# Performance work log

Measured on AMD Instinct MI355X. Metric: run time of the kernel, lower is better.

The kernel has to match this reference:

```python
import jax, jax.numpy as jnp
import numpy as np

B, S, E, N, H = 2, 2048, 2048, 16, 128  # batch, seq, embed, heads, depth


def sine_table(features, length, min_timescale=1.0, max_timescale=10000.0):
    fraction = jnp.arange(0, features, 2, dtype=jnp.float32) / features
    timescale = min_timescale * (max_timescale / min_timescale) ** fraction
    sinusoid_inp = jnp.einsum('i,j->ij', jnp.arange(length, dtype=jnp.float32), 1.0 / timescale,
                              precision=jax.lax.Precision.HIGHEST)
    sinusoid_inp = jnp.concatenate([sinusoid_inp, sinusoid_inp], axis=-1)  # [L, features]
    return jnp.sin(sinusoid_inp), jnp.cos(sinusoid_inp)


def rotate_half(x):
    x1, x2 = jnp.split(x, 2, axis=-1)
    return jnp.concatenate([-x2, x1], axis=-1)


def apply_rotary(q, k, cos, sin):
    # q: [B,S,N,H], k: [B,T,N,H]; cos/sin: [L,H] broadcast over (seq, depth)
    qcos = cos[: q.shape[1]][None, :, None, :]
    qsin = sin[: q.shape[1]][None, :, None, :]
    kcos = cos[: k.shape[1]][None, :, None, :]
    ksin = sin[: k.shape[1]][None, :, None, :]
    return q * qcos + rotate_half(q) * qsin, k * kcos + rotate_half(k) * ksin


def setup_inputs() -> dict:
    key = jax.random.key(0)
    ks = jax.random.split(key, 6)
    scale = 1.0 / np.sqrt(E)
    return {
        'x_q': jax.random.normal(ks[0], (B, S, E), jnp.float32),
        'x_kv': jax.random.normal(ks[1], (B, S, E), jnp.float32),
        'WQ': jax.random.normal(ks[2], (E, N, H), jnp.float32) * scale,
        'WK': jax.random.normal(ks[3], (E, N, H), jnp.float32) * scale,
        'WV': jax.random.normal(ks[4], (E, N, H), jnp.float32) * scale,
        'WO': jax.random.normal(ks[5], (N, H, E), jnp.float32) * scale,
    }


def reference(x_q, x_kv, WQ, WK, WV, WO):
    q = jnp.einsum('bse,enh->bsnh', x_q, WQ)
    k = jnp.einsum('bte,enh->btnh', x_kv, WK)
    v = jnp.einsum('bte,enh->btnh', x_kv, WV)

    sin, cos = sine_table(q.shape[-1], max(q.shape[1], k.shape[1]))
    q, k = apply_rotary(q, k, cos, sin)

    # causal attention bias: [1,1,S,T]
    s_len, t_len = q.shape[1], k.shape[1]
    causal = jnp.arange(s_len)[:, None] >= jnp.arange(t_len)[None, :]
    bias = jnp.where(causal, 0.0, -1e10).astype(jnp.float32)[None, None]

    logits = jnp.einsum('bsnh,btnh->bnst', q, k) / np.sqrt(H) + bias
    probs = jax.nn.softmax(logits, axis=-1)
    a = jnp.einsum('bnst,btnh->bsnh', probs, v)
    o = jnp.einsum('bsnh,nhe->bse', a, WO)
    return o
```

## Files before the change

kernel.cpp:

```cpp
#include <hip/hip_runtime.h>
#include <hip/hip_bf16.h>

typedef __bf16 bf16;
typedef __attribute__((ext_vector_type(8))) __bf16 bf16x8;
typedef __attribute__((ext_vector_type(4))) __bf16 bf16x4;
typedef __attribute__((ext_vector_type(4))) float f32x4;

typedef const __attribute__((address_space(1))) void* gptr_t;
typedef __attribute__((address_space(3))) void* sptr_t;

__device__ __forceinline__ void gload16(const void* g, void* l) {
  __builtin_amdgcn_global_load_lds((gptr_t)g, (sptr_t)l, 16, 0, 0);
}

#define MFMA_BF16(a, b, c) __builtin_amdgcn_mfma_f32_16x16x32_bf16((a), (b), (c), 0, 0, 0)

#define BAR() do { asm volatile("" ::: "memory"); __builtin_amdgcn_s_barrier(); asm volatile("" ::: "memory"); } while (0)

__device__ __forceinline__ int swzb(int l) { return l ^ (((l >> 7) & 7) << 4); }

namespace {
constexpr int kB = 2, kS = 2048, kE = 2048, kN = 16, kH = 128;
constexpr float kScale = 0.08838834764831845f;
constexpr float kLog2e = 1.4426950408889634f;
}

__global__ void k_cvt2(const float* __restrict__ a, const float* __restrict__ b,
                       bf16* __restrict__ oa, bf16* __restrict__ ob) {
  int bid = blockIdx.x;
  const float* in = (bid < 8192) ? a : b;
  bf16* out = (bid < 8192) ? oa : ob;
  int i = (bid & 8191) * 256 + threadIdx.x;
  float4 v = reinterpret_cast<const float4*>(in)[i];
  bf16x4 o = { (bf16)v.x, (bf16)v.y, (bf16)v.z, (bf16)v.w };
  reinterpret_cast<bf16x4*>(out)[i] = o;
}

__global__ void k_tconv4(const float* __restrict__ WQ, const float* __restrict__ WK,
                         const float* __restrict__ WV, const float* __restrict__ WO,
                         bf16* __restrict__ OQ, bf16* __restrict__ OK2,
                         bf16* __restrict__ OV, bf16* __restrict__ OO) {
  __shared__ float tile[64][68];
  int bid = blockIdx.x;
  int sel = bid >> 10;
  const float* in = (sel == 0) ? WQ : (sel == 1) ? WK : (sel == 2) ? WV : WO;
  bf16* out = (sel == 0) ? OQ : (sel == 1) ? OK2 : (sel == 2) ? OV : OO;
  int lb = bid & 1023;
  int bx = lb & 31, by = lb >> 5;
  int r0 = by * 64, c0 = bx * 64;
  int t = threadIdx.x;
  int rr = t >> 4, c4 = (t & 15) * 4;
#pragma unroll
  for (int k = 0; k < 4; ++k) {
    int r = rr + k * 16;
    float4 v = *reinterpret_cast<const float4*>(&in[(size_t)(r0 + r) * 2048 + c0 + c4]);
    tile[r][c4] = v.x; tile[r][c4 + 1] = v.y; tile[r][c4 + 2] = v.z; tile[r][c4 + 3] = v.w;
  }
  __syncthreads();
  int cc0 = t >> 3, r8 = (t & 7) * 8;
#pragma unroll
  for (int k = 0; k < 2; ++k) {
    int cc = cc0 + k * 32;
    bf16x8 o;
#pragma unroll
    for (int j = 0; j < 8; ++j) o[j] = (bf16)tile[r8 + j][cc];
    *reinterpret_cast<bf16x8*>(&out[(size_t)(c0 + cc) * 2048 + r0 + r8]) = o;
  }
}

__global__ void k_vtrans(const bf16* __restrict__ V, bf16* __restrict__ Vt) {
  __shared__ bf16 tile[64][72];
  int bid = blockIdx.x;
  int bn = bid >> 6;
  int s0 = ((bid >> 1) & 31) * 64;
  int h0 = (bid & 1) * 64;
  size_t base = (size_t)bn * kS * kH;
  int t = threadIdx.x;
  int r = t >> 3, c8 = (t & 7) * 8;
#pragma unroll
  for (int k = 0; k < 2; ++k) {
    int rr = r + k * 32;
    *reinterpret_cast<bf16x8*>(&tile[rr][c8]) =
        *reinterpret_cast<const bf16x8*>(&V[base + (size_t)(s0 + rr) * kH + h0 + c8]);
  }
  __syncthreads();
  int hh0 = t >> 3, s8 = (t & 7) * 8;
#pragma unroll
  for (int k = 0; k < 2; ++k) {
    int hh = hh0 + k * 32;
    bf16x8 o;
#pragma unroll
    for (int j = 0; j < 8; ++j) o[j] = tile[s8 + j][hh];
    *reinterpret_cast<bf16x8*>(&Vt[base + (size_t)(h0 + hh) * kS + s0 + s8]) = o;
  }
}

__global__ void k_trig(float* __restrict__ ctab, float* __restrict__ stab) {
  int tid = blockIdx.x * 256 + threadIdx.x;
  int s = tid >> 6, i = tid & 63;
  float inv = exp2f(-(float)i * 0.20762050593046457f);
  float ang = (float)s * inv;
  float sn, cs;
  sincosf(ang, &sn, &cs);
  ctab[tid] = cs;
  stab[tid] = sn;
}

__global__ void k_rope(bf16* __restrict__ Qd, bf16* __restrict__ Kd,
                       const float* __restrict__ ctab, const float* __restrict__ stab) {
  int tid = blockIdx.x * 256 + threadIdx.x;
  int i8 = (tid & 7) * 8;
  int s = (tid >> 3) & (kS - 1);
  int bn = tid >> 14;
  size_t base = ((size_t)bn * kS + s) * kH;
  float4 c0 = *reinterpret_cast<const float4*>(&ctab[(s << 6) + i8]);
  float4 c1 = *reinterpret_cast<const float4*>(&ctab[(s << 6) + i8 + 4]);
  float4 s0 = *reinterpret_cast<const float4*>(&stab[(s << 6) + i8]);
  float4 s1 = *reinterpret_cast<const float4*>(&stab[(s << 6) + i8 + 4]);
  float cs[8] = {c0.x, c0.y, c0.z, c0.w, c1.x, c1.y, c1.z, c1.w};
  float sn[8] = {s0.x, s0.y, s0.z, s0.w, s1.x, s1.y, s1.z, s1.w};
  bf16x8 qlo = *reinterpret_cast<const bf16x8*>(&Qd[base + i8]);
  bf16x8 qhi = *reinterpret_cast<const bf16x8*>(&Qd[base + 64 + i8]);
  bf16x8 klo = *reinterpret_cast<const bf16x8*>(&Kd[base + i8]);
  bf16x8 khi = *reinterpret_cast<const bf16x8*>(&Kd[base + 64 + i8]);
  bf16x8 qlo2, qhi2, klo2, khi2;
#pragma unroll
  for (int j = 0; j < 8; ++j) {
    float q1 = (float)qlo[j], q2 = (float)qhi[j];
    qlo2[j] = (bf16)(q1 * cs[j] - q2 * sn[j]);
    qhi2[j] = (bf16)(q2 * cs[j] + q1 * sn[j]);
    float k1 = (float)klo[j], k2 = (float)khi[j];
    klo2[j] = (bf16)(k1 * cs[j] - k2 * sn[j]);
    khi2[j] = (bf16)(k2 * cs[j] + k1 * sn[j]);
  }
  *reinterpret_cast<bf16x8*>(&Qd[base + i8]) = qlo2;
  *reinterpret_cast<bf16x8*>(&Qd[base + 64 + i8]) = qhi2;
  *reinterpret_cast<bf16x8*>(&Kd[base + i8]) = klo2;
  *reinterpret_cast<bf16x8*>(&Kd[base + 64 + i8]) = khi2;
}


__device__ __forceinline__ void stage_half(const bf16* __restrict__ src, size_t row0,
                                           int k0, char* slot, int t) {
#pragma unroll
  for (int i = 0; i < 2; ++i) {
    int idx = i * 512 + t;
    int d = idx * 16;
    int lb = d ^ (((d >> 7) & 7) << 4);
    int r = lb >> 7;
    int kc = (lb & 127) >> 1;
    gload16(src + (row0 + r) * 2048 + k0 + kc,
            slot + i * 8192 + (t >> 6) * 1024);
  }
}

#define AS1(b)    ((char*)LDS + (b) * 16384)
#define BS1(q, h) ((char*)LDS + 32768 + (q) * 32768 + (h) * 16384)

template <int MODE>
__global__ __launch_bounds__(512, 2) void k_gemm8(const bf16* __restrict__ Aq,
                                                  const bf16* __restrict__ Akv,
                                                  const bf16* __restrict__ Bt,
                                                  void* __restrict__ Cout) {
  constexpr int NTN = (MODE == 0) ? 24 : 8;
  constexpr int NTM = 32;
  constexpr int NT = 32;
  __shared__ __align__(16) char LDS[131072];
  int bid = blockIdx.x;
  constexpr int nblk = NTM * NTN;
  int swz = (bid & 7) * (nblk >> 3) + (bid >> 3);
  int mt = swz / NTN, nt = swz - mt * NTN;
  size_t m0 = (size_t)mt * 128;
  int n0 = nt * 256;
  const bf16* A = (MODE == 0 && nt >= 8) ? Akv : Aq;
  int t = threadIdx.x, wid = t >> 6, lane = t & 63;
  int l16 = lane & 15, lq = lane >> 4;
  int wr = wid >> 2, wc = wid & 3;
  int bhalf = wc >> 1;
  int brow0 = ((wc & 1) << 6) + l16;

  f32x4 acc[4][4] = {};
  bf16x8 af[4], bfr[4];

  stage_half(Bt, (size_t)n0,       0, BS1(0, 0), t);
  stage_half(Bt, (size_t)n0 + 128, 0, BS1(0, 1), t);
  stage_half(A,  m0,               0, AS1(0), t);
  stage_half(Bt, (size_t)n0,      64, BS1(1, 0), t);
  stage_half(Bt, (size_t)n0 + 128, 64, BS1(1, 1), t);
  asm volatile("s_waitcnt vmcnt(4)" ::: "memory");
  BAR();

  int bql = 0;
  for (int kt = 0; kt < NT; ++kt) {
    char* Ab = AS1(kt & 1);
    char* Anb = AS1((kt & 1) ^ 1);
    char* Bb = BS1(bql, bhalf);
    int bq2 = bql + 2; if (bq2 >= 3) bq2 -= 3;
#pragma unroll
    for (int j = 0; j < 4; ++j) {
      int l = (((wr * 4 + j) * 16 + l16) << 7) + (lq << 4);
      af[j] = *(const bf16x8*)(Ab + swzb(l));
    }
#pragma unroll
    for (int nf = 0; nf < 2; ++nf) {
      int l = ((brow0 + nf * 16) << 7) + (lq << 4);
      bfr[nf] = *(const bf16x8*)(Bb + swzb(l));
    }
    if (kt + 1 < NT) stage_half(A, m0, (kt + 1) * 64, Anb, t);
    BAR();
    __builtin_amdgcn_s_setprio(1);
#pragma unroll
    for (int j = 0; j < 4; ++j)
#pragma unroll
      for (int nf = 0; nf < 2; ++nf)
        acc[j][nf] = MFMA_BF16(af[j], bfr[nf], acc[j][nf]);
    __builtin_amdgcn_s_setprio(0);
    BAR();
#pragma unroll
    for (int nf = 0; nf < 2; ++nf) {
      int l = ((brow0 + (nf + 2) * 16) << 7) + (lq << 4);
      bfr[2 + nf] = *(const bf16x8*)(Bb + swzb(l));
    }
    if (kt + 2 < NT) {
      stage_half(Bt, (size_t)n0,       (kt + 2) * 64, BS1(bq2, 0), t);
      stage_half(Bt, (size_t)n0 + 128, (kt + 2) * 64, BS1(bq2, 1), t);
    }
    BAR();
    __builtin_amdgcn_s_setprio(1);
#pragma unroll
    for (int j = 0; j < 4; ++j)
#pragma unroll
      for (int nf = 0; nf < 2; ++nf)
        acc[j][2 + nf] = MFMA_BF16(af[j], bfr[2 + nf], acc[j][2 + nf]);
    __builtin_amdgcn_s_setprio(0);
    BAR();
#pragma unroll
    for (int j = 0; j < 4; ++j) {
      int l = (((wr * 4 + j) * 16 + l16) << 7) + 64 + (lq << 4);
      af[j] = *(const bf16x8*)(Ab + swzb(l));
    }
#pragma unroll
    for (int nf = 0; nf < 2; ++nf) {
      int l = ((brow0 + nf * 16) << 7) + 64 + (lq << 4);
      bfr[nf] = *(const bf16x8*)(Bb + swzb(l));
    }
    BAR();
    __builtin_amdgcn_s_setprio(1);
#pragma unroll
    for (int j = 0; j < 4; ++j)
#pragma unroll
      for (int nf = 0; nf < 2; ++nf)
        acc[j][nf] = MFMA_BF16(af[j], bfr[nf], acc[j][nf]);
    __builtin_amdgcn_s_setprio(0);
    BAR();
#pragma unroll
    for (int nf = 0; nf < 2; ++nf) {
      int l = ((brow0 + (nf + 2) * 16) << 7) + 64 + (lq << 4);
      bfr[2 + nf] = *(const bf16x8*)(Bb + swzb(l));
    }
    BAR();
    __builtin_amdgcn_s_setprio(1);
#pragma unroll
    for (int j = 0; j < 4; ++j)
#pragma unroll
      for (int nf = 0; nf < 2; ++nf)
        acc[j][2 + nf] = MFMA_BF16(af[j], bfr[2 + nf], acc[j][2 + nf]);
    __builtin_amdgcn_s_setprio(0);
    if (kt < NT - 2)       asm volatile("s_waitcnt vmcnt(4)" ::: "memory");
    else if (kt == NT - 2) asm volatile("s_waitcnt vmcnt(0)" ::: "memory");
    BAR();
    bql += 1; if (bql >= 3) bql -= 3;
  }

#pragma unroll
  for (int mf = 0; mf < 4; ++mf) {
    int rowb = (int)m0 + wr * 64 + mf * 16 + lq * 4;
#pragma unroll
    for (int nf = 0; nf < 4; ++nf) {
      int col = n0 + wc * 64 + nf * 16 + l16;
#pragma unroll
      for (int r = 0; r < 4; ++r) {
        float v = acc[mf][nf][r];
        int mrow = rowb + r;
        if (MODE == 0) {
          int grp = col >> 11, cw = col & 2047;
          int b = mrow >> 11, s = mrow & 2047, n = cw >> 7, h = cw & 127;
          ((bf16*)Cout)[(size_t)grp * 8388608 +
                        (((size_t)(b * 16 + n) * 2048 + s) << 7) + h] = (bf16)v;
        } else {
          ((float*)Cout)[((size_t)mrow << 11) + col] = v;
        }
      }
    }
  }
}

__global__ __launch_bounds__(512, 4) void k_attn(const bf16* __restrict__ Q,
                                                 const bf16* __restrict__ Kg,
                                                 const bf16* __restrict__ Vt,
                                                 bf16* __restrict__ AO) {
  __shared__ __align__(16) bf16 Ks[64 * 128];
  __shared__ __align__(16) bf16 Vs[128 * 64];
  __shared__ __align__(16) bf16 Ps[8][16][72];
  int bid = blockIdx.x;
  int half = bid >> 8;
  int bn = (half << 4) | ((bid >> 4) & 15);
  int qt = (bid & 15) ^ (half ? 15 : 0);
  int q0 = qt * 128;
  int t = threadIdx.x, wid = t >> 6, lane = t & 63;
  int l16 = lane & 15, lq = lane >> 4;
  size_t bnSH = (size_t)bn * kS * kH;

  int qrow_a = q0 + wid * 16 + l16;
  bf16x8 qf[4];
#pragma unroll
  for (int ks = 0; ks < 4; ++ks)
    qf[ks] = *(const bf16x8*)(Q + bnSH + (size_t)qrow_a * kH + ks * 32 + lq * 8);

  f32x4 oacc[8] = {};
  float mrun[4], lrun[4];
#pragma unroll
  for (int r = 0; r < 4; ++r) { mrun[r] = -1e30f; lrun[r] = 0.f; }

  int ntiles = (q0 + 128) >> 6;
  for (int kt = 0; kt < ntiles; ++kt) {
    int kv0 = kt * 64;
#pragma unroll
    for (int i = 0; i < 2; ++i) {
      int idx = i * 512 + t;
      {
        int row = idx >> 4, ch = idx & 15;
        int gch = ch ^ (row & 7);
        gload16(Kg + bnSH + (size_t)(kv0 + row) * kH + gch * 8,
                (char*)Ks + i * 8192 + wid * 1024);
      }
      {
        int row = idx >> 3, ch = idx & 7;
        int gch = ch ^ (row & 7);
        gload16(Vt + bnSH + (size_t)row * kS + kv0 + gch * 8,
                (char*)Vs + i * 8192 + wid * 1024);
      }
    }
    __syncthreads();

    f32x4 sacc[4] = {};
#pragma unroll
    for (int ks = 0; ks < 4; ++ks) {
#pragma unroll
      for (int ni = 0; ni < 4; ++ni) {
        int sp = ni * 16 + l16;
        int hb = (ks * 32 + lq * 8) * 2;
        bf16x8 kb = *(const bf16x8*)((const char*)Ks + sp * 256 + (hb ^ ((sp & 7) << 4)));
        sacc[ni] = MFMA_BF16(qf[ks], kb, sacc[ni]);
      }
    }

    bool need_mask = (kv0 + 63) > (q0 + wid * 16);
#pragma unroll
    for (int ni = 0; ni < 4; ++ni) {
      f32x4 v = sacc[ni] * kScale;
      if (need_mask) {
#pragma unroll
        for (int r = 0; r < 4; ++r) {
          int qrow = q0 + wid * 16 + lq * 4 + r;
          int col = kv0 + ni * 16 + l16;
          if (col > qrow) v[r] = -1e30f;
        }
      }
      sacc[ni] = v;
    }

    float pmv[4];
#pragma unroll
    for (int r = 0; r < 4; ++r) {
      float pm = fmaxf(fmaxf(sacc[0][r], sacc[1][r]),
                       fmaxf(sacc[2][r], sacc[3][r]));
      pm = fmaxf(pm, __shfl_xor(pm, 1));
      pm = fmaxf(pm, __shfl_xor(pm, 2));
      pm = fmaxf(pm, __shfl_xor(pm, 4));
      pm = fmaxf(pm, __shfl_xor(pm, 8));
      pmv[r] = pm;
    }
    bool growl = (pmv[0] > mrun[0] + 8.f) | (pmv[1] > mrun[1] + 8.f) |
                 (pmv[2] > mrun[2] + 8.f) | (pmv[3] > mrun[3] + 8.f);
    if (__any(growl)) {
#pragma unroll
      for (int r = 0; r < 4; ++r) {
        float mnew = fmaxf(mrun[r], pmv[r]);
        float alpha = exp2f((mrun[r] - mnew) * kLog2e);
        mrun[r] = mnew;
        lrun[r] *= alpha;
#pragma unroll
        for (int nj = 0; nj < 8; ++nj) oacc[nj][r] *= alpha;
      }
    }
#pragma unroll
    for (int r = 0; r < 4; ++r) {
      float rs = 0.f;
#pragma unroll
      for (int ni = 0; ni < 4; ++ni) {
        float p = exp2f((sacc[ni][r] - mrun[r]) * kLog2e);
        sacc[ni][r] = p;
        rs += p;
      }
      rs += __shfl_xor(rs, 1);
      rs += __shfl_xor(rs, 2);
      rs += __shfl_xor(rs, 4);
      rs += __shfl_xor(rs, 8);
      lrun[r] += rs;
    }

#pragma unroll
    for (int ni = 0; ni < 4; ++ni)
#pragma unroll
      for (int r = 0; r < 4; ++r)
        Ps[wid][lq * 4 + r][ni * 16 + l16] = (bf16)sacc[ni][r];

#pragma unroll
    for (int ks = 0; ks < 2; ++ks) {
      bf16x8 pa = *(const bf16x8*)&Ps[wid][l16][ks * 32 + lq * 8];
#pragma unroll
      for (int nj = 0; nj < 8; ++nj) {
        int h = nj * 16 + l16;
        int sb = (ks * 64 + lq * 16) ^ ((h & 7) << 4);
        bf16x8 vb = *(const bf16x8*)((const char*)Vs + h * 128 + sb);
        oacc[nj] = MFMA_BF16(pa, vb, oacc[nj]);
      }
    }
    __syncthreads();
  }

  int b = bn >> 4, n = bn & 15;
#pragma unroll
  for (int r = 0; r < 4; ++r) {
    float inv = 1.0f / lrun[r];
    int qrow = q0 + wid * 16 + lq * 4 + r;
#pragma unroll
    for (int nj = 0; nj < 8; ++nj) {
      float v = oacc[nj][r] * inv;
      AO[(((size_t)b * kS + qrow) * kN + n) * kH + nj * 16 + l16] = (bf16)v;
    }
  }
}

extern "C" void kernel_launch(void* const* d_in, const int* in_sizes, int n_in,
                              void* d_out, int out_size, void* d_ws, size_t ws_size,
                              hipStream_t stream) {
  (void)in_sizes; (void)n_in; (void)out_size; (void)ws_size;
  const float* x_q  = (const float*)d_in[0];
  const float* x_kv = (const float*)d_in[1];
  const float* WQ   = (const float*)d_in[2];
  const float* WK   = (const float*)d_in[3];
  const float* WV   = (const float*)d_in[4];
  const float* WO   = (const float*)d_in[5];
  float* out = (float*)d_out;
  char* w = (char*)d_ws;
  const size_t MB = 1ull << 20;
  bf16* xq  = (bf16*)(w + 0 * MB);
  bf16* xkv = (bf16*)(w + 16 * MB);
  bf16* WqT = (bf16*)(w + 32 * MB);
  bf16* WkT = (bf16*)(w + 40 * MB);
  bf16* WvT = (bf16*)(w + 48 * MB);
  bf16* WoT = (bf16*)(w + 56 * MB);
  bf16* Qb  = (bf16*)(w + 64 * MB);
  bf16* Kb  = (bf16*)(w + 80 * MB);
  bf16* Vb  = (bf16*)(w + 96 * MB);
  float* ctab = (float*)(w + 0 * MB);
  float* stab = (float*)(w + 1 * MB);
  bf16* AO  = xq;
  bf16* Vtb = xkv;

  k_cvt2<<<16384, 256, 0, stream>>>(x_q, x_kv, xq, xkv);
  k_tconv4<<<4096, 256, 0, stream>>>(WQ, WK, WV, WO, WqT, WkT, WvT, WoT);
  k_gemm8<0><<<768, 512, 0, stream>>>(xq, xkv, WqT, Qb);
  k_trig<<<512, 256, 0, stream>>>(ctab, stab);
  k_rope<<<2048, 256, 0, stream>>>(Qb, Kb, ctab, stab);
  k_vtrans<<<2048, 256, 0, stream>>>(Vb, Vtb);
  k_attn<<<512, 512, 0, stream>>>(Qb, Kb, Vtb, AO);
  k_gemm8<1><<<256, 512, 0, stream>>>(AO, AO, WoT, out);
}
```

Before: 438.7 us.

## Fuse V transpose into projection GEMM epilogue and register-prefetch attention K/V tiles

The projection GEMM now writes the V slice already transposed, staging it through LDS in its epilogue, so the separate V-transpose kernel and its global round trip go away. The attention kernel swaps direct global-to-LDS loads for register prefetch of the next K/V tile, which overlaps those global loads with the current tile's MFMA work. In exchange it uses more registers and adds an extra barrier per iteration, and the GEMM epilogue reuses LDS after a sync.

Result: slower. 464.5 us (+5.9%).

```diff
diff --git a/kernel.cpp b/kernel.cpp
--- a/kernel.cpp
+++ b/kernel.cpp
@@ -65,33 +65,6 @@
 #pragma unroll
     for (int j = 0; j < 8; ++j) o[j] = (bf16)tile[r8 + j][cc];
     *reinterpret_cast<bf16x8*>(&out[(size_t)(c0 + cc) * 2048 + r0 + r8]) = o;
-  }
-}
-
-__global__ void k_vtrans(const bf16* __restrict__ V, bf16* __restrict__ Vt) {
-  __shared__ bf16 tile[64][72];
-  int bid = blockIdx.x;
-  int bn = bid >> 6;
-  int s0 = ((bid >> 1) & 31) * 64;
-  int h0 = (bid & 1) * 64;
-  size_t base = (size_t)bn * kS * kH;
-  int t = threadIdx.x;
-  int r = t >> 3, c8 = (t & 7) * 8;
-#pragma unroll
-  for (int k = 0; k < 2; ++k) {
-    int rr = r + k * 32;
-    *reinterpret_cast<bf16x8*>(&tile[rr][c8]) =
-        *reinterpret_cast<const bf16x8*>(&V[base + (size_t)(s0 + rr) * kH + h0 + c8]);
-  }
-  __syncthreads();
-  int hh0 = t >> 3, s8 = (t & 7) * 8;
-#pragma unroll
-  for (int k = 0; k < 2; ++k) {
-    int hh = hh0 + k * 32;
-    bf16x8 o;
-#pragma unroll
-    for (int j = 0; j < 8; ++j) o[j] = tile[s8 + j][hh];
-    *reinterpret_cast<bf16x8*>(&Vt[base + (size_t)(h0 + hh) * kS + s0 + s8]) = o;
   }
 }
 
@@ -272,23 +245,53 @@
     bql += 1; if (bql >= 3) bql -= 3;
   }
 
-#pragma unroll
-  for (int mf = 0; mf < 4; ++mf) {
-    int rowb = (int)m0 + wr * 64 + mf * 16 + lq * 4;
-#pragma unroll
-    for (int nf = 0; nf < 4; ++nf) {
-      int col = n0 + wc * 64 + nf * 16 + l16;
-#pragma unroll
-      for (int r = 0; r < 4; ++r) {
-        float v = acc[mf][nf][r];
-        int mrow = rowb + r;
-        if (MODE == 0) {
-          int grp = col >> 11, cw = col & 2047;
-          int b = mrow >> 11, s = mrow & 2047, n = cw >> 7, h = cw & 127;
-          ((bf16*)Cout)[(size_t)grp * 8388608 +
-                        (((size_t)(b * 16 + n) * 2048 + s) << 7) + h] = (bf16)v;
-        } else {
-          ((float*)Cout)[((size_t)mrow << 11) + col] = v;
+  if (MODE == 0 && n0 >= 4096) {
+    __syncthreads();
+    char* myT = (char*)LDS + wid * 9216;
+#pragma unroll
+    for (int mf = 0; mf < 4; ++mf)
+#pragma unroll
+      for (int nf = 0; nf < 4; ++nf) {
+        bf16x4 v4;
+#pragma unroll
+        for (int r = 0; r < 4; ++r) v4[r] = (bf16)acc[mf][nf][r];
+        int hh = nf * 16 + l16;
+        int ss = mf * 16 + lq * 4;
+        *(bf16x4*)(myT + hh * 144 + ss * 2) = v4;
+      }
+    int cw = (n0 - 4096) + wc * 64;
+    int n = cw >> 7;
+    int h0w = cw & 127;
+    int mrow0 = (int)m0 + wr * 64;
+    int b = mrow0 >> 11, s0w = mrow0 & 2047;
+    bf16* VtO = (bf16*)Cout + (size_t)2 * 8388608;
+    size_t base = ((size_t)(b * 16 + n)) * 262144;
+#pragma unroll
+    for (int j = 0; j < 8; ++j) {
+      int u = j * 64 + lane;
+      int hh = u >> 3, sb = u & 7;
+      uint4 val = *(const uint4*)(myT + hh * 144 + sb * 16);
+      *(uint4*)(VtO + base + (size_t)(h0w + hh) * 2048 + s0w + sb * 8) = val;
+    }
+  } else {
+#pragma unroll
+    for (int mf = 0; mf < 4; ++mf) {
+      int rowb = (int)m0 + wr * 64 + mf * 16 + lq * 4;
+#pragma unroll
+      for (int nf = 0; nf < 4; ++nf) {
+        int col = n0 + wc * 64 + nf * 16 + l16;
+#pragma unroll
+        for (int r = 0; r < 4; ++r) {
+          float v = acc[mf][nf][r];
+          int mrow = rowb + r;
+          if (MODE == 0) {
+            int grp = col >> 11, cw = col & 2047;
+            int b = mrow >> 11, s = mrow & 2047, n = cw >> 7, h = cw & 127;
+            ((bf16*)Cout)[(size_t)grp * 8388608 +
+                          (((size_t)(b * 16 + n) * 2048 + s) << 7) + h] = (bf16)v;
+          } else {
+            ((float*)Cout)[((size_t)mrow << 11) + col] = v;
+          }
         }
       }
     }
@@ -322,26 +325,34 @@
 #pragma unroll
   for (int r = 0; r < 4; ++r) { mrun[r] = -1e30f; lrun[r] = 0.f; }
 
+  uint4 kreg[2], vreg[2];
+  auto LOADREGS = [&](int kv0) {
+#pragma unroll
+    for (int i = 0; i < 2; ++i) {
+      int u = i * 512 + t;
+      kreg[i] = *(const uint4*)(Kg + bnSH + (size_t)(kv0 + (u >> 4)) * kH + (u & 15) * 8);
+      vreg[i] = *(const uint4*)(Vt + bnSH + (size_t)(u >> 3) * kS + kv0 + (u & 7) * 8);
+    }
+  };
+  auto WRITEREGS = [&]() {
+#pragma unroll
+    for (int i = 0; i < 2; ++i) {
+      int u = i * 512 + t;
+      int row = u >> 4, sl = u & 15;
+      *(uint4*)((char*)Ks + row * 256 + ((sl * 16) ^ ((row & 7) << 4))) = kreg[i];
+      int h = u >> 3, s8 = u & 7;
+      *(uint4*)((char*)Vs + h * 128 + ((s8 * 16) ^ ((h & 7) << 4))) = vreg[i];
+    }
+  };
+
   int ntiles = (q0 + 128) >> 6;
+  LOADREGS(0);
+  WRITEREGS();
+  __syncthreads();
+
   for (int kt = 0; kt < ntiles; ++kt) {
     int kv0 = kt * 64;
-#pragma unroll
-    for (int i = 0; i < 2; ++i) {
-      int idx = i * 512 + t;
-      {
-        int row = idx >> 4, ch = idx & 15;
-        int gch = ch ^ (row & 7);
-        gload16(Kg + bnSH + (size_t)(kv0 + row) * kH + gch * 8,
-                (char*)Ks + i * 8192 + wid * 1024);
-      }
-      {
-        int row = idx >> 3, ch = idx & 7;
-        int gch = ch ^ (row & 7);
-        gload16(Vt + bnSH + (size_t)row * kS + kv0 + gch * 8,
-                (char*)Vs + i * 8192 + wid * 1024);
-      }
-    }
-    __syncthreads();
+    if (kt + 1 < ntiles) LOADREGS(kv0 + 64);
 
     f32x4 sacc[4] = {};
 #pragma unroll
@@ -427,7 +438,12 @@
         oacc[nj] = MFMA_BF16(pa, vb, oacc[nj]);
       }
     }
-    __syncthreads();
+
+    if (kt + 1 < ntiles) {
+      __syncthreads();
+      WRITEREGS();
+      __syncthreads();
+    }
   }
 
   int b = bn >> 4, n = bn & 15;
@@ -464,18 +480,16 @@
   bf16* WoT = (bf16*)(w + 56 * MB);
   bf16* Qb  = (bf16*)(w + 64 * MB);
   bf16* Kb  = (bf16*)(w + 80 * MB);
-  bf16* Vb  = (bf16*)(w + 96 * MB);
+  bf16* Vtb = (bf16*)(w + 96 * MB);
   float* ctab = (float*)(w + 0 * MB);
   float* stab = (float*)(w + 1 * MB);
   bf16* AO  = xq;
-  bf16* Vtb = xkv;
 
   k_cvt2<<<16384, 256, 0, stream>>>(x_q, x_kv, xq, xkv);
   k_tconv4<<<4096, 256, 0, stream>>>(WQ, WK, WV, WO, WqT, WkT, WvT, WoT);
   k_gemm8<0><<<768, 512, 0, stream>>>(xq, xkv, WqT, Qb);
   k_trig<<<512, 256, 0, stream>>>(ctab, stab);
   k_rope<<<2048, 256, 0, stream>>>(Qb, Kb, ctab, stab);
-  k_vtrans<<<2048, 256, 0, stream>>>(Vb, Vtb);
   k_attn<<<512, 512, 0, stream>>>(Qb, Kb, Vtb, AO);
   k_gemm8<1><<<256, 512, 0, stream>>>(AO, AO, WoT, out);
 }
```
